# Optimization experiments

Hardware: AMD Instinct MI355X
Metric: run time of the kernel (lower is better)

## Reference

```python
import jax, jax.numpy as jnp
import numpy as np

N = 50000        # nodes
E = 1_600_000    # edges
IN = 64          # in_channels
HID = 16         # hidden_dim (per-head channels)
HEADS = 8
OUT = 32         # out_channels
B = 256          # graphs in batch
NEG_SLOPE = 0.2  # PyG GATv2Conv default


def gatv2_conv(x, edge_index, wl, bl, wr, br, att, bias, heads, ch, concat, num_nodes):
    """Faithful GATv2Conv (PyG semantics, eval mode, add self-loops disabled upstream
    is not the case in PyG default, but the module uses default add_self_loops=True;
    we add them here)."""
    src, dst = edge_index[0], edge_index[1]
    # PyG default add_self_loops=True
    loop = jnp.arange(num_nodes, dtype=src.dtype)
    src = jnp.concatenate([src, loop])
    dst = jnp.concatenate([dst, loop])
    xl = (x @ wl + bl).reshape(num_nodes, heads, ch)  # source transform
    xr = (x @ wr + br).reshape(num_nodes, heads, ch)  # target transform
    # per-edge GATv2 score: att . leaky_relu(xl[src] + xr[dst])
    e = jax.nn.leaky_relu(xl[src] + xr[dst], NEG_SLOPE)          # [E, H, C]
    logits = jnp.einsum('ehc,hc->eh', e, att)                     # [E, H]
    # segment softmax over incoming edges of each dst node (max detached, as in PyG)
    m = jax.lax.stop_gradient(jax.ops.segment_max(logits, dst, num_segments=num_nodes))
    a = jnp.exp(logits - m[dst])
    denom = jax.ops.segment_sum(a, dst, num_segments=num_nodes)
    alpha = a / (denom[dst] + 1e-16)                              # [E, H]
    msg = xl[src] * alpha[..., None]                              # [E, H, C]
    out = jax.ops.segment_sum(msg, dst, num_segments=num_nodes)   # [N, H, C]
    if concat:
        out = out.reshape(num_nodes, heads * ch) + bias
    else:
        out = out.mean(axis=1) + bias
    return out


def global_mean_pool(x, batch, num_graphs):
    s = jax.ops.segment_sum(x, batch, num_segments=num_graphs)
    cnt = jax.ops.segment_sum(jnp.ones((x.shape[0],), x.dtype), batch, num_segments=num_graphs)
    return s / jnp.maximum(cnt, 1.0)[:, None]


def setup_inputs() -> dict:
    key = jax.random.key(0)
    ks = jax.random.split(key, 24)
    f32 = jnp.float32
    def g(k, shape, s=0.1):
        return jax.random.normal(k, shape, f32) * s
    inp = {
        'x': jax.random.normal(ks[0], (N, IN), f32),
        'edge_index': jax.random.randint(ks[1], (2, E), 0, N, dtype=jnp.int32),
        'batch': jnp.sort(jax.random.randint(ks[2], (N,), 0, B, dtype=jnp.int32)),
        # conv1: GATv2Conv(IN -> HID, heads=HEADS, concat=True)
        'wl1': g(ks[3], (IN, HEADS * HID)), 'bl1': jnp.zeros((HEADS * HID,), f32),
        'wr1': g(ks[4], (IN, HEADS * HID)), 'br1': jnp.zeros((HEADS * HID,), f32),
        'att1': g(ks[5], (HEADS, HID)),
        'bias1': jnp.zeros((HEADS * HID,), f32),
        # conv2: GATv2Conv(HEADS*HID -> HID, heads=1, concat=False)
        'wl2': g(ks[6], (HEADS * HID, HID)), 'bl2': jnp.zeros((HID,), f32),
        'wr2': g(ks[7], (HEADS * HID, HID)), 'br2': jnp.zeros((HID,), f32),
        'att2': g(ks[8], (1, HID)),
        'bias2': jnp.zeros((HID,), f32),
        # MLP: HID -> 2*HID -> HID -> OUT
        'w_m1': g(ks[9], (HID, 2 * HID)), 'b_m1': jnp.zeros((2 * HID,), f32),
        'w_m2': g(ks[10], (2 * HID, HID)), 'b_m2': jnp.zeros((HID,), f32),
        'w_m3': g(ks[11], (HID, OUT)), 'b_m3': jnp.zeros((OUT,), f32),
    }
    return inp


def reference(x, edge_index, batch,
              wl1, bl1, wr1, br1, att1, bias1,
              wl2, bl2, wr2, br2, att2, bias2,
              w_m1, b_m1, w_m2, b_m2, w_m3, b_m3):
    # eval mode: all dropouts are identity
    h = jax.nn.elu(gatv2_conv(x, edge_index, wl1, bl1, wr1, br1, att1, bias1,
                              HEADS, HID, True, N))
    h = jax.nn.elu(gatv2_conv(h, edge_index, wl2, bl2, wr2, br2, att2, bias2,
                              1, HID, False, N))
    h = global_mean_pool(h, batch, B)                 # [B, HID]
    h = jax.nn.elu(h @ w_m1 + b_m1)
    h = jax.nn.elu(h @ w_m2 + b_m2)
    return h @ w_m3 + b_m3                            # [B, OUT]
```

## Files before the change

### kernel.cpp

```cpp
#include <hip/hip_runtime.h>
#include <hip/hip_bf16.h>
#include <hip/hip_fp16.h>
#include <math.h>

#define NN   50000
#define NE   1600000
#define EP   (NE + NN)
#define NB   256
#define BK_SH 6
#define BKN  (1 << BK_SH)
#define NBKT ((NN + BKN - 1) >> BK_SH)
#define CAP_SH 12
#define CAP  (1 << CAP_SH)
#define ET   32
#define EB   (256 * ET)
#define EBLK ((NE + EB - 1) / EB)

__device__ __forceinline__ float elu_f(float x)   { return x > 0.0f ? x : expm1f(x); }
__device__ __forceinline__ float lrelu_f(float x) { return fmaxf(x, 0.2f * x); }

__global__ __launch_bounds__(256) void k_gemm1(
    const float* __restrict__ x, const float* __restrict__ wl,
    const float* __restrict__ bl, const float* __restrict__ wr,
    const float* __restrict__ br, __half* __restrict__ xl1, float* __restrict__ xr1)
{
    __shared__ float xs[32 * 64];
    const int tid = threadIdx.x;
    const int n0  = blockIdx.x * 32;
    const int nrem = min(32, NN - n0);

    const float4* xg = (const float4*)(x + (size_t)n0 * 64);
    float4* xs4 = (float4*)xs;
    const int lim4 = nrem * 16;
    for (int i = tid; i < lim4; i += 256) xs4[i] = xg[i];
    __syncthreads();

    const int g  = tid >> 6;
    const int c0 = (tid & 63) * 4;
    const bool isl = (c0 < 128);
    const float* w  = isl ? wl : wr;
    const float* b  = isl ? bl : br;
    const int    cw = isl ? c0 : (c0 - 128);

    float4 acc[8];
#pragma unroll
    for (int r = 0; r < 8; ++r) acc[r] = make_float4(0.f, 0.f, 0.f, 0.f);

    for (int k4 = 0; k4 < 16; ++k4) {
        const float4 w0 = *(const float4*)&w[(k4*4+0)*128 + cw];
        const float4 w1 = *(const float4*)&w[(k4*4+1)*128 + cw];
        const float4 w2 = *(const float4*)&w[(k4*4+2)*128 + cw];
        const float4 w3 = *(const float4*)&w[(k4*4+3)*128 + cw];
#pragma unroll
        for (int r = 0; r < 8; ++r) {
            const float4 xv = xs4[(g*8+r)*16 + k4];
            acc[r].x += xv.x*w0.x + xv.y*w1.x + xv.z*w2.x + xv.w*w3.x;
            acc[r].y += xv.x*w0.y + xv.y*w1.y + xv.z*w2.y + xv.w*w3.y;
            acc[r].z += xv.x*w0.z + xv.y*w1.z + xv.z*w2.z + xv.w*w3.z;
            acc[r].w += xv.x*w0.w + xv.y*w1.w + xv.z*w2.w + xv.w*w3.w;
        }
    }
    const float4 bv = *(const float4*)&b[cw];
#pragma unroll
    for (int r = 0; r < 8; ++r) {
        const int row = g*8 + r;
        if (row < nrem) {
            float4 o = make_float4(acc[r].x + bv.x, acc[r].y + bv.y,
                                   acc[r].z + bv.z, acc[r].w + bv.w);
            if (isl) {
                __half2* dst = (__half2*)&xl1[(size_t)(n0 + row) * 128 + cw];
                dst[0] = __floats2half2_rn(o.x, o.y);
                dst[1] = __floats2half2_rn(o.z, o.w);
            } else {
                *(float4*)&xr1[(size_t)(n0 + row) * 128 + cw] = o;
            }
        }
    }
}

__global__ void k_binit(int* __restrict__ bcursor)
{
    int i = blockIdx.x * 256 + threadIdx.x;
    if (i < NBKT) bcursor[i] = i << CAP_SH;
}

__global__ __launch_bounds__(256) void k_bucket(const int* __restrict__ ei,
                                                int* __restrict__ bcursor,
                                                unsigned int* __restrict__ bb)
{
    __shared__ int lh[NBKT];
    __shared__ int cur[NBKT];
    const int tid = threadIdx.x;
    for (int i = tid; i < NBKT; i += 256) lh[i] = 0;
    __syncthreads();

    const int t = blockIdx.x * 256 + tid;
    const bool act = (t * ET < NE);
    int4 dreg[ET / 4];
    if (act) {
        const int4* dp = (const int4*)&ei[NE + t * ET];
#pragma unroll
        for (int q = 0; q < ET / 4; ++q) {
            dreg[q] = dp[q];
            atomicAdd(&lh[dreg[q].x >> BK_SH], 1);
            atomicAdd(&lh[dreg[q].y >> BK_SH], 1);
            atomicAdd(&lh[dreg[q].z >> BK_SH], 1);
            atomicAdd(&lh[dreg[q].w >> BK_SH], 1);
        }
    }
    __syncthreads();
    for (int i = tid; i < NBKT; i += 256) {
        int h = lh[i];
        if (h > 0) cur[i] = atomicAdd(&bcursor[i], h);
    }
    __syncthreads();
    if (act) {
        const int4* sp = (const int4*)&ei[t * ET];
#pragma unroll
        for (int q = 0; q < ET / 4; ++q) {
            int4 s = sp[q];
            int4 d = dreg[q];
            int bkt, p;
            bkt = d.x >> BK_SH; p = atomicAdd(&cur[bkt], 1);
            if (p < ((bkt + 1) << CAP_SH))
                bb[p] = ((unsigned)(d.x & (BKN-1)) << 17) | (unsigned)s.x;
            bkt = d.y >> BK_SH; p = atomicAdd(&cur[bkt], 1);
            if (p < ((bkt + 1) << CAP_SH))
                bb[p] = ((unsigned)(d.y & (BKN-1)) << 17) | (unsigned)s.y;
            bkt = d.z >> BK_SH; p = atomicAdd(&cur[bkt], 1);
            if (p < ((bkt + 1) << CAP_SH))
                bb[p] = ((unsigned)(d.z & (BKN-1)) << 17) | (unsigned)s.z;
            bkt = d.w >> BK_SH; p = atomicAdd(&cur[bkt], 1);
            if (p < ((bkt + 1) << CAP_SH))
                bb[p] = ((unsigned)(d.w & (BKN-1)) << 17) | (unsigned)s.w;
        }
    }
}

__global__ __launch_bounds__(1024) void k_bscan(const int* __restrict__ bcursor,
                                                int* __restrict__ bstart)
{
    __shared__ int sm[1024];
    const int t = threadIdx.x;
    const int c = (t < NBKT) ? (bcursor[t] - (t << CAP_SH)) : 0;
    sm[t] = c;
    __syncthreads();
    for (int ofs = 1; ofs < 1024; ofs <<= 1) {
        int v = (t >= ofs) ? sm[t - ofs] : 0;
        __syncthreads();
        sm[t] += v;
        __syncthreads();
    }
    if (t < NBKT) bstart[t] = sm[t] - c;
    if (t == NBKT) bstart[NBKT] = NE;
}

__global__ __launch_bounds__(256) void k_bfinal(
    const unsigned int* __restrict__ bb, const int* __restrict__ bstart,
    int* __restrict__ rowp, int* __restrict__ slist)
{
    __shared__ int cnt[BKN], cur[BKN];
    const int b = blockIdx.x, tid = threadIdx.x;
    const int db0 = b << BK_SH;
    const int dn  = min(BKN, NN - db0);
    const int ebeg = bstart[b];
    const int count = bstart[b + 1] - ebeg;
    const unsigned int* src = bb + ((size_t)b << CAP_SH);
    const int out0 = ebeg + db0;

    int c0 = 0;
    if (tid < BKN) {
        c0 = (tid < dn) ? 1 : 0;
        cnt[tid] = c0;
    }
    __syncthreads();
    for (int i = tid; i < count; i += 256)
        atomicAdd(&cnt[src[i] >> 17], 1);
    __syncthreads();
    if (tid < BKN) c0 = cnt[tid];
    for (int ofs = 1; ofs < BKN; ofs <<= 1) {
        int v = 0;
        if (tid < BKN && tid >= ofs) v = cnt[tid - ofs];
        __syncthreads();
        if (tid < BKN) cnt[tid] += v;
        __syncthreads();
    }
    if (tid < BKN) {
        int ex = cnt[tid] - c0;
        cur[tid] = ex + 1;
        if (tid < dn) {
            rowp[db0 + tid] = out0 + ex;
            slist[out0 + ex] = db0 + tid;
        }
    }
    if (b == 0 && tid == 0) rowp[NN] = EP;
    __syncthreads();
    for (int i = tid; i < count; i += 256) {
        unsigned u = src[i];
        int p = atomicAdd(&cur[u >> 17], 1);
        slist[out0 + p] = (int)(u & 0x1FFFFu);
    }
}

__global__ __launch_bounds__(256) void k_conv1_agg(
    const __half* __restrict__ xl1, const float* __restrict__ xr1,
    const float* __restrict__ att, const float* __restrict__ bias1,
    const int* __restrict__ rowp, const int* __restrict__ slist,
    float* __restrict__ h1)
{
    const int d = (blockIdx.x * 256 + threadIdx.x) >> 6;
    if (d >= NN) return;
    const int lane = threadIdx.x & 63;
    const int h = lane >> 3, e = lane & 7;
    const int cb = h * 16;

    float xrv[16], atv[16];
    {
        const float4* xrp = (const float4*)&xr1[(size_t)d * 128 + cb];
        const float4* atp = (const float4*)&att[cb];
#pragma unroll
        for (int q = 0; q < 4; ++q) {
            float4 a4 = xrp[q];
            xrv[q*4+0] = a4.x; xrv[q*4+1] = a4.y; xrv[q*4+2] = a4.z; xrv[q*4+3] = a4.w;
            float4 b4 = atp[q];
            atv[q*4+0] = b4.x; atv[q*4+1] = b4.y; atv[q*4+2] = b4.z; atv[q*4+3] = b4.w;
        }
    }

    const int beg = rowp[d], end = rowp[d + 1];

    float den = 0.f;
    float a[16];
#pragma unroll
    for (int c = 0; c < 16; ++c) a[c] = 0.f;

    for (int base = beg; base < end; base += 64) {
        const int nb = min(64, end - base);
        int sv = (lane < nb) ? slist[base + lane] : 0;
        for (int c8 = 0; c8 * 8 < nb; ++c8) {
            const int idx = c8 * 8 + e;
            const int src = __shfl(sv, idx);
            if (idx < nb) {
                const float4* vp = (const float4*)(xl1 + (size_t)src * 128 + cb);
                const float4 r0 = vp[0], r1 = vp[1];
                float v[16];
                {
                    const __half2* hh = (const __half2*)&r0;
#pragma unroll
                    for (int q = 0; q < 4; ++q) {
                        float2 f = __half22float2(hh[q]);
                        v[2*q] = f.x; v[2*q+1] = f.y;
                    }
                    const __half2* hg = (const __half2*)&r1;
#pragma unroll
                    for (int q = 0; q < 4; ++q) {
                        float2 f = __half22float2(hg[q]);
                        v[8+2*q] = f.x; v[9+2*q] = f.y;
                    }
                }
                float s = 0.f;
#pragma unroll
                for (int c = 0; c < 16; ++c) s += atv[c] * lrelu_f(v[c] + xrv[c]);
                const float w = __expf(fminf(s, 80.f));
                den += w;
#pragma unroll
                for (int c = 0; c < 16; ++c) a[c] += w * v[c];
            }
        }
    }

    den += __shfl_xor(den, 1);
    den += __shfl_xor(den, 2);
    den += __shfl_xor(den, 4);

    const bool b0 = (e & 1), b1 = (e & 2), b2 = (e & 4);
    float t1[8], u1[8];
#pragma unroll
    for (int j = 0; j < 8; ++j) {
        t1[j] = b0 ? a[j + 8] : a[j];
        u1[j] = b0 ? a[j] : a[j + 8];
    }
#pragma unroll
    for (int j = 0; j < 8; ++j) t1[j] += __shfl_xor(u1[j], 1);
    float t2[4], u2[4];
#pragma unroll
    for (int j = 0; j < 4; ++j) {
        t2[j] = b1 ? t1[j + 4] : t1[j];
        u2[j] = b1 ? t1[j] : t1[j + 4];
    }
#pragma unroll
    for (int j = 0; j < 4; ++j) t2[j] += __shfl_xor(u2[j], 2);
    float t3[2], u3[2];
#pragma unroll
    for (int j = 0; j < 2; ++j) {
        t3[j] = b2 ? t2[j + 2] : t2[j];
        u3[j] = b2 ? t2[j] : t2[j + 2];
    }
#pragma unroll
    for (int j = 0; j < 2; ++j) t3[j] += __shfl_xor(u3[j], 4);

    const int c0 = (b0 ? 8 : 0) + (b1 ? 4 : 0) + (b2 ? 2 : 0);
    const float inv = 1.0f / (den + 1e-16f);
    const int c = cb + c0;
    const float o0 = elu_f(t3[0] * inv + bias1[c]);
    const float o1 = elu_f(t3[1] * inv + bias1[c + 1]);
    *(float2*)&h1[(size_t)d * 128 + c] = make_float2(o0, o1);
}

__global__ __launch_bounds__(256) void k_gemm2(
    const float* __restrict__ h1, const float* __restrict__ wl,
    const float* __restrict__ bl, const float* __restrict__ wr,
    const float* __restrict__ br, __half* __restrict__ xl2, float* __restrict__ xr2)
{
    __shared__ float xs[32 * 132];
    const int tid = threadIdx.x;
    const int n0  = blockIdx.x * 32;
    const int nrem = min(32, NN - n0);

    for (int i = tid; i < nrem * 128; i += 256) {
        int row = i >> 7, col = i & 127;
        xs[row * 132 + col] = h1[(size_t)(n0 + row) * 128 + col];
    }
    __syncthreads();

    const int r  = tid >> 3;
    const int c0 = (tid & 7) * 4;
    const bool isl = (c0 < 16);
    const float* w = isl ? wl : wr;
    const float* b = isl ? bl : br;
    const int    c = isl ? c0 : (c0 - 16);

    float4 acc = make_float4(0.f, 0.f, 0.f, 0.f);
    for (int k4 = 0; k4 < 32; ++k4) {
        const float4 w0 = *(const float4*)&w[(k4*4+0)*16 + c];
        const float4 w1 = *(const float4*)&w[(k4*4+1)*16 + c];
        const float4 w2 = *(const float4*)&w[(k4*4+2)*16 + c];
        const float4 w3 = *(const float4*)&w[(k4*4+3)*16 + c];
        const float4 xv = *(const float4*)&xs[r * 132 + k4 * 4];
        acc.x += xv.x*w0.x + xv.y*w1.x + xv.z*w2.x + xv.w*w3.x;
        acc.y += xv.x*w0.y + xv.y*w1.y + xv.z*w2.y + xv.w*w3.y;
        acc.z += xv.x*w0.z + xv.y*w1.z + xv.z*w2.z + xv.w*w3.z;
        acc.w += xv.x*w0.w + xv.y*w1.w + xv.z*w2.w + xv.w*w3.w;
    }
    if (r < nrem) {
        const float4 bv = *(const float4*)&b[c];
        float4 o = make_float4(acc.x + bv.x, acc.y + bv.y, acc.z + bv.z, acc.w + bv.w);
        if (isl) {
            __half2* dst = (__half2*)&xl2[(size_t)(n0 + r) * 16 + c];
            dst[0] = __floats2half2_rn(o.x, o.y);
            dst[1] = __floats2half2_rn(o.z, o.w);
        } else {
            *(float4*)&xr2[(size_t)(n0 + r) * 16 + c] = o;
        }
    }
}

__global__ __launch_bounds__(256) void k_conv2_agg(
    const __half* __restrict__ xl2, const float* __restrict__ xr2,
    const float* __restrict__ att, const float* __restrict__ bias2,
    const int* __restrict__ rowp, const int* __restrict__ slist,
    float* __restrict__ h2)
{
    const int d = (blockIdx.x * 256 + threadIdx.x) >> 6;
    if (d >= NN) return;
    const int lane = threadIdx.x & 63;
    const int eq = lane >> 2, c4 = lane & 3;

    const float4 xr = *(const float4*)&xr2[(size_t)d * 16 + c4 * 4];
    const float4 at = *(const float4*)&att[c4 * 4];
    const int beg = rowp[d], end = rowp[d + 1];

    float den = 0.f;
    float4 acc = make_float4(0.f, 0.f, 0.f, 0.f);

    for (int base = beg; base < end; base += 64) {
        const int nb = min(64, end - base);
        int sv = (lane < nb) ? slist[base + lane] : 0;
        for (int c16 = 0; c16 * 16 < nb; ++c16) {
            const int idx = c16 * 16 + eq;
            const int src = __shfl(sv, idx & 63);
            if (idx < nb) {
                const __half2* hp = (const __half2*)(xl2 + (size_t)src * 16 + c4 * 4);
                const float2 f0 = __half22float2(hp[0]);
                const float2 f1 = __half22float2(hp[1]);
                float pp = at.x * lrelu_f(f0.x + xr.x)
                         + at.y * lrelu_f(f0.y + xr.y)
                         + at.z * lrelu_f(f1.x + xr.z)
                         + at.w * lrelu_f(f1.y + xr.w);
                pp += __shfl_xor(pp, 1);
                pp += __shfl_xor(pp, 2);
                const float w = __expf(fminf(pp, 80.f));
                den += w;
                acc.x += w * f0.x;
                acc.y += w * f0.y;
                acc.z += w * f1.x;
                acc.w += w * f1.y;
            }
        }
    }
#pragma unroll
    for (int ofs = 4; ofs < 64; ofs <<= 1) {
        den   += __shfl_xor(den, ofs);
        acc.x += __shfl_xor(acc.x, ofs);
        acc.y += __shfl_xor(acc.y, ofs);
        acc.z += __shfl_xor(acc.z, ofs);
        acc.w += __shfl_xor(acc.w, ofs);
    }
    if (eq == 0) {
        const float inv = 1.0f / (den + 1e-16f);
        const float4 bv = *(const float4*)&bias2[c4 * 4];
        float4 o;
        o.x = elu_f(acc.x * inv + bv.x);
        o.y = elu_f(acc.y * inv + bv.y);
        o.z = elu_f(acc.z * inv + bv.z);
        o.w = elu_f(acc.w * inv + bv.w);
        *(float4*)&h2[(size_t)d * 16 + c4 * 4] = o;
    }
}

__global__ __launch_bounds__(256) void k_pool(
    const float* __restrict__ h2, const int* __restrict__ batch,
    float* __restrict__ pooled, float* __restrict__ cnt)
{
    __shared__ int se[2];
    __shared__ float sm[256];
    const int b = blockIdx.x, tid = threadIdx.x;
    if (tid < 2) {
        int key = b + tid, lo = 0, hi = NN;
        while (lo < hi) {
            int mid = (lo + hi) >> 1;
            if (batch[mid] < key) lo = mid + 1; else hi = mid;
        }
        se[tid] = lo;
    }
    __syncthreads();
    const int s = se[0], e = se[1];
    const int c = tid & 15, slot = tid >> 4;
    float acc = 0.f;
    for (int n = s + slot; n < e; n += 16) acc += h2[(size_t)n * 16 + c];
    sm[tid] = acc;
    __syncthreads();
    for (int ofs = 128; ofs >= 16; ofs >>= 1) {
        if (tid < ofs) sm[tid] += sm[tid + ofs];
        __syncthreads();
    }
    if (tid < 16) pooled[b * 16 + tid] = sm[tid];
    if (tid == 16) cnt[b] = (float)(e - s);
}

__global__ __launch_bounds__(256) void k_mlp(
    const float* __restrict__ pooled, const float* __restrict__ cnt,
    const float* __restrict__ w1, const float* __restrict__ b1,
    const float* __restrict__ w2, const float* __restrict__ b2,
    const float* __restrict__ w3, const float* __restrict__ b3,
    float* __restrict__ out)
{
    __shared__ float w1s[16*32], w2s[32*16], w3s[16*32], b1s[32], b2s[16], b3s[32];
    const int tid = threadIdx.x;
    for (int i = tid; i < 512; i += 256) { w1s[i] = w1[i]; w2s[i] = w2[i]; w3s[i] = w3[i]; }
    if (tid < 32) b1s[tid] = b1[tid];
    if (tid < 16) b2s[tid] = b2[tid];
    if (tid < 32) b3s[tid] = b3[tid];
    __syncthreads();

    const int g = tid;
    const float inv = 1.0f / fmaxf(cnt[g], 1.0f);
    float hb[16];
#pragma unroll
    for (int k = 0; k < 16; ++k) hb[k] = pooled[g * 16 + k] * inv;

    float t1[32];
#pragma unroll
    for (int j = 0; j < 32; ++j) t1[j] = b1s[j];
    for (int k = 0; k < 16; ++k)
#pragma unroll
        for (int j = 0; j < 32; ++j) t1[j] += hb[k] * w1s[k * 32 + j];
#pragma unroll
    for (int j = 0; j < 32; ++j) t1[j] = elu_f(t1[j]);

    float t2[16];
#pragma unroll
    for (int j = 0; j < 16; ++j) t2[j] = b2s[j];
    for (int k = 0; k < 32; ++k)
#pragma unroll
        for (int j = 0; j < 16; ++j) t2[j] += t1[k] * w2s[k * 16 + j];
#pragma unroll
    for (int j = 0; j < 16; ++j) t2[j] = elu_f(t2[j]);

#pragma unroll
    for (int j = 0; j < 32; ++j) {
        float o = b3s[j];
        for (int k = 0; k < 16; ++k) o += t2[k] * w3s[k * 32 + j];
        out[g * 32 + j] = o;
    }
}

extern "C" void kernel_launch(void* const* d_in, const int* in_sizes, int n_in,
                              void* d_out, int out_size, void* d_ws, size_t ws_size,
                              hipStream_t stream)
{
    const float* x     = (const float*)d_in[0];
    const int*   ei    = (const int*)d_in[1];
    const int*   batch = (const int*)d_in[2];
    const float* wl1   = (const float*)d_in[3];
    const float* bl1   = (const float*)d_in[4];
    const float* wr1   = (const float*)d_in[5];
    const float* br1   = (const float*)d_in[6];
    const float* att1  = (const float*)d_in[7];
    const float* bias1 = (const float*)d_in[8];
    const float* wl2   = (const float*)d_in[9];
    const float* bl2   = (const float*)d_in[10];
    const float* wr2   = (const float*)d_in[11];
    const float* br2   = (const float*)d_in[12];
    const float* att2  = (const float*)d_in[13];
    const float* bias2 = (const float*)d_in[14];
    const float* wm1   = (const float*)d_in[15];
    const float* bm1   = (const float*)d_in[16];
    const float* wm2   = (const float*)d_in[17];
    const float* bm2   = (const float*)d_in[18];
    const float* wm3   = (const float*)d_in[19];
    const float* bm3   = (const float*)d_in[20];
    float* out = (float*)d_out;

    char* base = (char*)d_ws;
    size_t off = 0;
    auto alloc = [&](size_t bytes) -> void* {
        void* p = base + off;
        off += (bytes + 255) & ~(size_t)255;
        return p;
    };
    __half* xl1  = (__half*)alloc((size_t)NN * 128 * 2);
    float* xr1   = (float*)alloc((size_t)NN * 128 * 4);
    float* h1    = (float*)alloc((size_t)NN * 128 * 4);
    int*   slist = (int*)  alloc((size_t)EP * 4);
    unsigned int* bb = (unsigned int*)alloc((size_t)NBKT * CAP * 4);
    int*   rowp  = (int*)  alloc((size_t)(NN + 1) * 4);
    int*   bstart= (int*)  alloc((size_t)(NBKT + 1) * 4);
    int*   bcursor=(int*)  alloc((size_t)NBKT * 4);
    __half* xl2  = (__half*)alloc((size_t)NN * 16 * 2);
    float* xr2   = (float*)alloc((size_t)NN * 16 * 4);
    float* h2    = (float*)alloc((size_t)NN * 16 * 4);
    float* pooled= (float*)alloc((size_t)NB * 16 * 4);
    float* cnt   = (float*)alloc((size_t)NB * 4);

    k_binit<<<(NBKT + 255) / 256, 256, 0, stream>>>(bcursor);
    k_gemm1<<<(NN + 31) / 32, 256, 0, stream>>>(x, wl1, bl1, wr1, br1, xl1, xr1);
    k_bucket<<<EBLK, 256, 0, stream>>>(ei, bcursor, bb);
    k_bscan<<<1, 1024, 0, stream>>>(bcursor, bstart);
    k_bfinal<<<NBKT, 256, 0, stream>>>(bb, bstart, rowp, slist);
    k_conv1_agg<<<(NN * 64) / 256, 256, 0, stream>>>(xl1, xr1, att1, bias1, rowp, slist, h1);
    k_gemm2<<<(NN + 31) / 32, 256, 0, stream>>>(h1, wl2, bl2, wr2, br2, xl2, xr2);
    k_conv2_agg<<<(NN * 64) / 256, 256, 0, stream>>>(xl2, xr2, att2, bias2, rowp, slist, h2);
    k_pool<<<NB, 256, 0, stream>>>(h2, batch, pooled, cnt);
    k_mlp<<<1, 256, 0, stream>>>(pooled, cnt, wm1, bm1, wm2, bm2, wm3, bm3, out);
}
```

Before: 340.7 us.

## Merge GEMM1 with edge bucketing and fold bucket scan into finalize

Launches the first-layer GEMM and the edge bucketing pass as one kernel, with block ranges split by blockIdx, so the two independent phases can overlap on the GPU. It also removes the separate single-block scan kernel: each finalize block computes its own bucket start offset by reducing the counts of all preceding buckets. This cuts two kernel launches and their serialization gaps, but each finalize block now re-reads up to roughly 780 bucket counters redundantly. The combined kernel also reserves shared memory for both phases in every block, which may lower occupancy.

```diff
diff --git a/kernel.cpp b/kernel.cpp
--- a/kernel.cpp
+++ b/kernel.cpp
@@ -15,156 +15,150 @@
 #define ET   32
 #define EB   (256 * ET)
 #define EBLK ((NE + EB - 1) / EB)
+#define G1   ((NN + 31) / 32)
 
 __device__ __forceinline__ float elu_f(float x)   { return x > 0.0f ? x : expm1f(x); }
 __device__ __forceinline__ float lrelu_f(float x) { return fmaxf(x, 0.2f * x); }
 
-__global__ __launch_bounds__(256) void k_gemm1(
+__global__ __launch_bounds__(256) void k_gemm1_bucket(
     const float* __restrict__ x, const float* __restrict__ wl,
     const float* __restrict__ bl, const float* __restrict__ wr,
-    const float* __restrict__ br, __half* __restrict__ xl1, float* __restrict__ xr1)
+    const float* __restrict__ br, __half* __restrict__ xl1, float* __restrict__ xr1,
+    const int* __restrict__ ei, int* __restrict__ bcursor,
+    unsigned int* __restrict__ bb)
 {
     __shared__ float xs[32 * 64];
-    const int tid = threadIdx.x;
-    const int n0  = blockIdx.x * 32;
-    const int nrem = min(32, NN - n0);
-
-    const float4* xg = (const float4*)(x + (size_t)n0 * 64);
-    float4* xs4 = (float4*)xs;
-    const int lim4 = nrem * 16;
-    for (int i = tid; i < lim4; i += 256) xs4[i] = xg[i];
-    __syncthreads();
-
-    const int g  = tid >> 6;
-    const int c0 = (tid & 63) * 4;
-    const bool isl = (c0 < 128);
-    const float* w  = isl ? wl : wr;
-    const float* b  = isl ? bl : br;
-    const int    cw = isl ? c0 : (c0 - 128);
-
-    float4 acc[8];
-#pragma unroll
-    for (int r = 0; r < 8; ++r) acc[r] = make_float4(0.f, 0.f, 0.f, 0.f);
-
-    for (int k4 = 0; k4 < 16; ++k4) {
-        const float4 w0 = *(const float4*)&w[(k4*4+0)*128 + cw];
-        const float4 w1 = *(const float4*)&w[(k4*4+1)*128 + cw];
-        const float4 w2 = *(const float4*)&w[(k4*4+2)*128 + cw];
-        const float4 w3 = *(const float4*)&w[(k4*4+3)*128 + cw];
-#pragma unroll
-        for (int r = 0; r < 8; ++r) {
-            const float4 xv = xs4[(g*8+r)*16 + k4];
-            acc[r].x += xv.x*w0.x + xv.y*w1.x + xv.z*w2.x + xv.w*w3.x;
-            acc[r].y += xv.x*w0.y + xv.y*w1.y + xv.z*w2.y + xv.w*w3.y;
-            acc[r].z += xv.x*w0.z + xv.y*w1.z + xv.z*w2.z + xv.w*w3.z;
-            acc[r].w += xv.x*w0.w + xv.y*w1.w + xv.z*w2.w + xv.w*w3.w;
-        }
-    }
-    const float4 bv = *(const float4*)&b[cw];
-#pragma unroll
-    for (int r = 0; r < 8; ++r) {
-        const int row = g*8 + r;
-        if (row < nrem) {
-            float4 o = make_float4(acc[r].x + bv.x, acc[r].y + bv.y,
-                                   acc[r].z + bv.z, acc[r].w + bv.w);
-            if (isl) {
-                __half2* dst = (__half2*)&xl1[(size_t)(n0 + row) * 128 + cw];
-                dst[0] = __floats2half2_rn(o.x, o.y);
-                dst[1] = __floats2half2_rn(o.z, o.w);
-            } else {
-                *(float4*)&xr1[(size_t)(n0 + row) * 128 + cw] = o;
-            }
-        }
-    }
-}
-
-__global__ void k_binit(int* __restrict__ bcursor)
-{
-    int i = blockIdx.x * 256 + threadIdx.x;
-    if (i < NBKT) bcursor[i] = i << CAP_SH;
-}
-
-__global__ __launch_bounds__(256) void k_bucket(const int* __restrict__ ei,
-                                                int* __restrict__ bcursor,
-                                                unsigned int* __restrict__ bb)
-{
     __shared__ int lh[NBKT];
     __shared__ int cur[NBKT];
     const int tid = threadIdx.x;
-    for (int i = tid; i < NBKT; i += 256) lh[i] = 0;
-    __syncthreads();
-
-    const int t = blockIdx.x * 256 + tid;
-    const bool act = (t * ET < NE);
-    int4 dreg[ET / 4];
-    if (act) {
-        const int4* dp = (const int4*)&ei[NE + t * ET];
-#pragma unroll
-        for (int q = 0; q < ET / 4; ++q) {
-            dreg[q] = dp[q];
-            atomicAdd(&lh[dreg[q].x >> BK_SH], 1);
-            atomicAdd(&lh[dreg[q].y >> BK_SH], 1);
-            atomicAdd(&lh[dreg[q].z >> BK_SH], 1);
-            atomicAdd(&lh[dreg[q].w >> BK_SH], 1);
-        }
-    }
-    __syncthreads();
-    for (int i = tid; i < NBKT; i += 256) {
-        int h = lh[i];
-        if (h > 0) cur[i] = atomicAdd(&bcursor[i], h);
-    }
-    __syncthreads();
-    if (act) {
-        const int4* sp = (const int4*)&ei[t * ET];
-#pragma unroll
-        for (int q = 0; q < ET / 4; ++q) {
-            int4 s = sp[q];
-            int4 d = dreg[q];
-            int bkt, p;
-            bkt = d.x >> BK_SH; p = atomicAdd(&cur[bkt], 1);
-            if (p < ((bkt + 1) << CAP_SH))
-                bb[p] = ((unsigned)(d.x & (BKN-1)) << 17) | (unsigned)s.x;
-            bkt = d.y >> BK_SH; p = atomicAdd(&cur[bkt], 1);
-            if (p < ((bkt + 1) << CAP_SH))
-                bb[p] = ((unsigned)(d.y & (BKN-1)) << 17) | (unsigned)s.y;
-            bkt = d.z >> BK_SH; p = atomicAdd(&cur[bkt], 1);
-            if (p < ((bkt + 1) << CAP_SH))
-                bb[p] = ((unsigned)(d.z & (BKN-1)) << 17) | (unsigned)s.z;
-            bkt = d.w >> BK_SH; p = atomicAdd(&cur[bkt], 1);
-            if (p < ((bkt + 1) << CAP_SH))
-                bb[p] = ((unsigned)(d.w & (BKN-1)) << 17) | (unsigned)s.w;
-        }
-    }
-}
-
-__global__ __launch_bounds__(1024) void k_bscan(const int* __restrict__ bcursor,
-                                                int* __restrict__ bstart)
-{
-    __shared__ int sm[1024];
-    const int t = threadIdx.x;
-    const int c = (t < NBKT) ? (bcursor[t] - (t << CAP_SH)) : 0;
-    sm[t] = c;
-    __syncthreads();
-    for (int ofs = 1; ofs < 1024; ofs <<= 1) {
-        int v = (t >= ofs) ? sm[t - ofs] : 0;
-        __syncthreads();
-        sm[t] += v;
-        __syncthreads();
-    }
-    if (t < NBKT) bstart[t] = sm[t] - c;
-    if (t == NBKT) bstart[NBKT] = NE;
+
+    if (blockIdx.x < G1) {
+        const int n0  = blockIdx.x * 32;
+        const int nrem = min(32, NN - n0);
+
+        const float4* xg = (const float4*)(x + (size_t)n0 * 64);
+        float4* xs4 = (float4*)xs;
+        const int lim4 = nrem * 16;
+        for (int i = tid; i < lim4; i += 256) xs4[i] = xg[i];
+        __syncthreads();
+
+        const int g  = tid >> 6;
+        const int c0 = (tid & 63) * 4;
+        const bool isl = (c0 < 128);
+        const float* w  = isl ? wl : wr;
+        const float* b  = isl ? bl : br;
+        const int    cw = isl ? c0 : (c0 - 128);
+
+        float4 acc[8];
+#pragma unroll
+        for (int r = 0; r < 8; ++r) acc[r] = make_float4(0.f, 0.f, 0.f, 0.f);
+
+        for (int k4 = 0; k4 < 16; ++k4) {
+            const float4 w0 = *(const float4*)&w[(k4*4+0)*128 + cw];
+            const float4 w1 = *(const float4*)&w[(k4*4+1)*128 + cw];
+            const float4 w2 = *(const float4*)&w[(k4*4+2)*128 + cw];
+            const float4 w3 = *(const float4*)&w[(k4*4+3)*128 + cw];
+#pragma unroll
+            for (int r = 0; r < 8; ++r) {
+                const float4 xv = xs4[(g*8+r)*16 + k4];
+                acc[r].x += xv.x*w0.x + xv.y*w1.x + xv.z*w2.x + xv.w*w3.x;
+                acc[r].y += xv.x*w0.y + xv.y*w1.y + xv.z*w2.y + xv.w*w3.y;
+                acc[r].z += xv.x*w0.z + xv.y*w1.z + xv.z*w2.z + xv.w*w3.z;
+                acc[r].w += xv.x*w0.w + xv.y*w1.w + xv.z*w2.w + xv.w*w3.w;
+            }
+        }
+        const float4 bv = *(const float4*)&b[cw];
+#pragma unroll
+        for (int r = 0; r < 8; ++r) {
+            const int row = g*8 + r;
+            if (row < nrem) {
+                float4 o = make_float4(acc[r].x + bv.x, acc[r].y + bv.y,
+                                       acc[r].z + bv.z, acc[r].w + bv.w);
+                if (isl) {
+                    __half2* dst = (__half2*)&xl1[(size_t)(n0 + row) * 128 + cw];
+                    dst[0] = __floats2half2_rn(o.x, o.y);
+                    dst[1] = __floats2half2_rn(o.z, o.w);
+                } else {
+                    *(float4*)&xr1[(size_t)(n0 + row) * 128 + cw] = o;
+                }
+            }
+        }
+    } else {
+        const int bid = blockIdx.x - G1;
+        for (int i = tid; i < NBKT; i += 256) lh[i] = 0;
+        __syncthreads();
+
+        const int t = bid * 256 + tid;
+        const bool act = (t * ET < NE);
+        int4 dreg[ET / 4];
+        if (act) {
+            const int4* dp = (const int4*)&ei[NE + t * ET];
+#pragma unroll
+            for (int q = 0; q < ET / 4; ++q) {
+                dreg[q] = dp[q];
+                atomicAdd(&lh[dreg[q].x >> BK_SH], 1);
+                atomicAdd(&lh[dreg[q].y >> BK_SH], 1);
+                atomicAdd(&lh[dreg[q].z >> BK_SH], 1);
+                atomicAdd(&lh[dreg[q].w >> BK_SH], 1);
+            }
+        }
+        __syncthreads();
+        for (int i = tid; i < NBKT; i += 256) {
+            int h = lh[i];
+            if (h > 0) cur[i] = atomicAdd(&bcursor[i], h);
+        }
+        __syncthreads();
+        if (act) {
+            const int4* sp = (const int4*)&ei[t * ET];
+#pragma unroll
+            for (int q = 0; q < ET / 4; ++q) {
+                int4 s = sp[q];
+                int4 d = dreg[q];
+                int bkt, p;
+                bkt = d.x >> BK_SH; p = atomicAdd(&cur[bkt], 1);
+                if (p < ((bkt + 1) << CAP_SH))
+                    bb[p] = ((unsigned)(d.x & (BKN-1)) << 17) | (unsigned)s.x;
+                bkt = d.y >> BK_SH; p = atomicAdd(&cur[bkt], 1);
+                if (p < ((bkt + 1) << CAP_SH))
+                    bb[p] = ((unsigned)(d.y & (BKN-1)) << 17) | (unsigned)s.y;
+                bkt = d.z >> BK_SH; p = atomicAdd(&cur[bkt], 1);
+                if (p < ((bkt + 1) << CAP_SH))
+                    bb[p] = ((unsigned)(d.z & (BKN-1)) << 17) | (unsigned)s.z;
+                bkt = d.w >> BK_SH; p = atomicAdd(&cur[bkt], 1);
+                if (p < ((bkt + 1) << CAP_SH))
+                    bb[p] = ((unsigned)(d.w & (BKN-1)) << 17) | (unsigned)s.w;
+            }
+        }
+    }
+}
+
+__global__ void k_binit(int* __restrict__ bcursor)
+{
+    int i = blockIdx.x * 256 + threadIdx.x;
+    if (i < NBKT) bcursor[i] = i << CAP_SH;
 }
 
 __global__ __launch_bounds__(256) void k_bfinal(
-    const unsigned int* __restrict__ bb, const int* __restrict__ bstart,
+    const unsigned int* __restrict__ bb, const int* __restrict__ bcursor,
     int* __restrict__ rowp, int* __restrict__ slist)
 {
     __shared__ int cnt[BKN], cur[BKN];
+    __shared__ int red[256];
     const int b = blockIdx.x, tid = threadIdx.x;
     const int db0 = b << BK_SH;
     const int dn  = min(BKN, NN - db0);
-    const int ebeg = bstart[b];
-    const int count = bstart[b + 1] - ebeg;
+
+    int part = 0;
+    for (int i = tid; i < b; i += 256)
+        part += min(bcursor[i] - (i << CAP_SH), CAP);
+    red[tid] = part;
+    __syncthreads();
+    for (int ofs = 128; ofs >= 1; ofs >>= 1) {
+        if (tid < ofs) red[tid] += red[tid + ofs];
+        __syncthreads();
+    }
+    const int ebeg = red[0];
+    const int count = min(bcursor[b] - (b << CAP_SH), CAP);
     const unsigned int* src = bb + ((size_t)b << CAP_SH);
     const int out0 = ebeg + db0;
 
@@ -535,7 +529,6 @@
     int*   slist = (int*)  alloc((size_t)EP * 4);
     unsigned int* bb = (unsigned int*)alloc((size_t)NBKT * CAP * 4);
     int*   rowp  = (int*)  alloc((size_t)(NN + 1) * 4);
-    int*   bstart= (int*)  alloc((size_t)(NBKT + 1) * 4);
     int*   bcursor=(int*)  alloc((size_t)NBKT * 4);
     __half* xl2  = (__half*)alloc((size_t)NN * 16 * 2);
     float* xr2   = (float*)alloc((size_t)NN * 16 * 4);
@@ -544,10 +537,9 @@
     float* cnt   = (float*)alloc((size_t)NB * 4);
 
     k_binit<<<(NBKT + 255) / 256, 256, 0, stream>>>(bcursor);
-    k_gemm1<<<(NN + 31) / 32, 256, 0, stream>>>(x, wl1, bl1, wr1, br1, xl1, xr1);
-    k_bucket<<<EBLK, 256, 0, stream>>>(ei, bcursor, bb);
-    k_bscan<<<1, 1024, 0, stream>>>(bcursor, bstart);
-    k_bfinal<<<NBKT, 256, 0, stream>>>(bb, bstart, rowp, slist);
+    k_gemm1_bucket<<<G1 + EBLK, 256, 0, stream>>>(x, wl1, bl1, wr1, br1, xl1, xr1,
+                                                  ei, bcursor, bb);
+    k_bfinal<<<NBKT, 256, 0, stream>>>(bb, bcursor, rowp, slist);
     k_conv1_agg<<<(NN * 64) / 256, 256, 0, stream>>>(xl1, xr1, att1, bias1, rowp, slist, h1);
     k_gemm2<<<(NN + 31) / 32, 256, 0, stream>>>(h1, wl2, bl2, wr2, br2, xl2, xr2);
     k_conv2_agg<<<(NN * 64) / 256, 256, 0, stream>>>(xl2, xr2, att2, bias2, rowp, slist, h2);
```

Result: faster. 323.8 us (-5.0%).
